# Performance work log

Measured on AMD Instinct MI355X. Metric: run time of the kernel, lower is better.

The kernel has to match this reference:

```python
import jax, jax.numpy as jnp
import numpy as np

H = 5  # hidden size of both LSTMs

def _lstm_layer(x, Wih, Whh, bih, bhh):
    """x: [B,T,I] -> hs: [B,T,H]. PyTorch gate order i,f,g,o; zero init state."""
    B, T, _ = x.shape
    # precompute input contribution for all timesteps: [T,B,4H]
    xg = (jnp.einsum('bti,gi->btg', x, Wih) + bih + bhh).transpose(1, 0, 2)
    def step(carry, xg_t):
        h, c = carry
        g = xg_t + h @ Whh.T
        i, f, gg, o = jnp.split(g, 4, axis=-1)
        c = jax.nn.sigmoid(f) * c + jax.nn.sigmoid(i) * jnp.tanh(gg)
        h = jax.nn.sigmoid(o) * jnp.tanh(c)
        return (h, c), h
    h0 = jnp.zeros((B, H), x.dtype)
    (_, _), hs = jax.lax.scan(step, (h0, h0), xg)
    return hs.transpose(1, 0, 2)  # [B,T,H]

def setup_inputs() -> dict:
    key = jax.random.key(0)
    ks = jax.random.split(key, 32)
    B, T = 16384, 128
    def u(k, shape, fan):
        s = 1.0 / np.sqrt(fan)
        return jax.random.uniform(k, shape, jnp.float32, -s, s)
    inp = {
        'x1': jax.random.normal(ks[0], (B, T, 5), jnp.float32),
        'x2': jax.random.normal(ks[1], (B, T, 5), jnp.float32),
        # lstm1 (1 layer)
        'Wih1': u(ks[2], (4*H, 5), H), 'Whh1': u(ks[3], (4*H, H), H),
        'bih1': u(ks[4], (4*H,), H), 'bhh1': u(ks[5], (4*H,), H),
        # lstm2 layer 0
        'Wih2a': u(ks[6], (4*H, 5), H), 'Whh2a': u(ks[7], (4*H, H), H),
        'bih2a': u(ks[8], (4*H,), H), 'bhh2a': u(ks[9], (4*H,), H),
        # lstm2 layer 1
        'Wih2b': u(ks[10], (4*H, H), H), 'Whh2b': u(ks[11], (4*H, H), H),
        'bih2b': u(ks[12], (4*H,), H), 'bhh2b': u(ks[13], (4*H,), H),
        # FC stack 20->32->32->16->16->5
        'W1': u(ks[14], (32, 20), 20), 'b1': u(ks[15], (32,), 20),
        'W2': u(ks[16], (32, 32), 32), 'b2': u(ks[17], (32,), 32),
        'W3': u(ks[18], (16, 32), 32), 'b3': u(ks[19], (16,), 32),
        'W4': u(ks[20], (16, 16), 16), 'b4': u(ks[21], (16,), 16),
        'W5': u(ks[22], (5, 16), 16), 'b5': u(ks[23], (5,), 16),
    }
    return inp

def reference(x1, x2, Wih1, Whh1, bih1, bhh1, Wih2a, Whh2a, bih2a, bhh2a,
              Wih2b, Whh2b, bih2b, bhh2b, W1, b1, W2, b2, W3, b3, W4, b4, W5, b5):
    out1 = _lstm_layer(x1, Wih1, Whh1, bih1, bhh1)[:, -1, :]            # [B,5]
    h2 = _lstm_layer(x2, Wih2a, Whh2a, bih2a, bhh2a)                    # [B,T,5]
    out2 = _lstm_layer(h2, Wih2b, Whh2b, bih2b, bhh2b)[:, -1, :]        # [B,5]
    out = jnp.concatenate([x1[:, -1, :], x2[:, -1, :], out1, out2], axis=1)  # [B,20]
    out = jax.nn.relu(out @ W1.T + b1)
    out = jax.nn.relu(out @ W2.T + b2)
    out = jax.nn.relu(out @ W3.T + b3)
    out = jax.nn.relu(out @ W4.T + b4)
    return out @ W5.T + b5  # [B,5]
```

## Files before the change

### kernel.cpp

```cpp
#include <hip/hip_runtime.h>

#define DEV __device__ __forceinline__
#define KSIG (-1.442695041f)
#define KTANH (-2.885390082f)

typedef float f2 __attribute__((ext_vector_type(2)));
typedef float f4 __attribute__((ext_vector_type(4)));

DEV float fexp2(float x) { return __builtin_amdgcn_exp2f(x); }
DEV float frcp(float x) { return __builtin_amdgcn_rcpf(x); }
DEV float bperm(int a, float x) {
  return __int_as_float(__builtin_amdgcn_ds_bpermute(a, __float_as_int(x)));
}
DEV f2 pkfma(f2 a, f2 b, f2 c) { return __builtin_elementwise_fma(a, b, c); }

struct CellP {
  f2 wx[4][2];
  f2 wh[4][2];
  float wx4[4], wh4[4];
  f2 b2[4];
};

DEV void load_cellP(CellP& W, int u, const float* __restrict__ Wih,
                    const float* __restrict__ Whh,
                    const float* __restrict__ bih,
                    const float* __restrict__ bhh) {
#pragma unroll
  for (int rt = 0; rt < 4; ++rt) {
    int row = 5 * rt + u;
    float kx = (rt == 2) ? KTANH : KSIG;
    W.wx[rt][0] = (f2){kx * Wih[row * 5 + 0], kx * Wih[row * 5 + 1]};
    W.wx[rt][1] = (f2){kx * Wih[row * 5 + 2], kx * Wih[row * 5 + 3]};
    W.wx4[rt] = kx * Wih[row * 5 + 4];
    W.wh[rt][0] = (f2){kx * Whh[row * 5 + 0], kx * Whh[row * 5 + 1]};
    W.wh[rt][1] = (f2){kx * Whh[row * 5 + 2], kx * Whh[row * 5 + 3]};
    W.wh4[rt] = kx * Whh[row * 5 + 4];
    W.b2[rt] = (f2){kx * (bih[row] + bhh[row]), 0.f};
  }
}

DEV float stepP(const CellP& W, const f2 xp[2], float x4, float hAll[5],
                float& c, const int bp[5]) {
  f2 hp0 = (f2){hAll[0], hAll[1]};
  f2 hp1 = (f2){hAll[2], hAll[3]};
  float acc[4];
#pragma unroll
  for (int rt = 0; rt < 4; ++rt) {
    f2 a2 = pkfma(W.wh[rt][0], hp0, W.b2[rt]);
    a2 = pkfma(W.wh[rt][1], hp1, a2);
    a2 = pkfma(W.wx[rt][0], xp[0], a2);
    a2 = pkfma(W.wx[rt][1], xp[1], a2);
    float a = a2.x + a2.y;
    a = fmaf(W.wh4[rt], hAll[4], a);
    acc[rt] = fmaf(W.wx4[rt], x4, a);
  }
  float gi = frcp(1.f + fexp2(acc[0]));
  float gf = frcp(1.f + fexp2(acc[1]));
  float gg = fmaf(2.f, frcp(1.f + fexp2(acc[2])), -1.f);
  float go = frcp(1.f + fexp2(acc[3]));
  c = fmaf(gf, c, gi * gg);
  float th = fmaf(2.f, frcp(1.f + fexp2(KTANH * c)), -1.f);
  float h = go * th;
#pragma unroll
  for (int u2 = 0; u2 < 5; ++u2) hAll[u2] = bperm(bp[u2], h);
  return h;
}

struct XBuf {
  f4 a, b, c, d, e;
};
DEV void xload(XBuf& bf, const float* __restrict__ px, int ch) {
  const f4* q = (const f4*)px + ch * 5;
  bf.a = q[0];
  bf.b = q[1];
  bf.c = q[2];
  bf.d = q[3];
  bf.e = q[4];
}

__global__ __launch_bounds__(192, 3) void rnn_a_kernel(
    const float* __restrict__ x1, const float* __restrict__ x2,
    const float* __restrict__ Wih1, const float* __restrict__ Whh1,
    const float* __restrict__ bih1, const float* __restrict__ bhh1,
    const float* __restrict__ Wih2a, const float* __restrict__ Whh2a,
    const float* __restrict__ bih2a, const float* __restrict__ bhh2a,
    float* __restrict__ h2a, float* __restrict__ h1l, int B, int N1) {
  const int tid = threadIdx.x;
  const int wid = blockIdx.x * 3 + (tid >> 6);
  if (wid >= 2 * N1) return;
  const int l = tid & 63;
  int g = l / 5;
  const int u = l - 5 * g;
  const bool act = (g < 12);
  if (!act) g = 11;
  const bool r2 = (wid >= N1);
  const int e = (r2 ? wid - N1 : wid) * 12 + g;
  const int ec = (e < B) ? e : B - 1;

  CellP W;
  if (r2)
    load_cellP(W, u, Wih2a, Whh2a, bih2a, bhh2a);
  else
    load_cellP(W, u, Wih1, Whh1, bih1, bhh1);

  int bp[5];
#pragma unroll
  for (int k = 0; k < 5; ++k) bp[k] = (5 * g + k) * 4;

  const float* px = (r2 ? x2 : x1) + (size_t)ec * 640;
  const bool wr = r2 && act && (e < B);
  float* ps = h2a + (size_t)ec * 640 + u;

  float hAll[5];
  float c = 0.f, hOwn = 0.f;
#pragma unroll
  for (int k = 0; k < 5; ++k) hAll[k] = 0.f;

#define SA1(S, xa, xb, xc, xd, xe)                  \
  {                                                 \
    f2 xin[2] = {(f2){xa, xb}, (f2){xc, xd}};       \
    hOwn = stepP(W, xin, xe, hAll, c, bp);          \
    if (wr) pst[(S) * 5] = hOwn;                    \
  }
#define CHUNKA(X)                                  \
  SA1(0, X.a.x, X.a.y, X.a.z, X.a.w, X.b.x)        \
  SA1(1, X.b.y, X.b.z, X.b.w, X.c.x, X.c.y)        \
  SA1(2, X.c.z, X.c.w, X.d.x, X.d.y, X.d.z)        \
  SA1(3, X.d.w, X.e.x, X.e.y, X.e.z, X.e.w)

  XBuf A0, B0;
  xload(A0, px, 0);
  for (int ch = 0; ch < 32; ch += 2) {
    xload(B0, px, (ch + 1 < 32) ? ch + 1 : 31);
    {
      float* pst = ps + (size_t)ch * 20;
      CHUNKA(A0);
    }
    xload(A0, px, (ch + 2 < 32) ? ch + 2 : 31);
    {
      float* pst = ps + (size_t)(ch + 1) * 20;
      CHUNKA(B0);
    }
  }
#undef SA1
#undef CHUNKA

  if (!r2 && act && e < B) h1l[(size_t)e * 5 + u] = hOwn;
}

__global__ __launch_bounds__(192, 2) void rnn_b_kernel(
    const float* __restrict__ x1, const float* __restrict__ x2,
    const float* __restrict__ Wih2b, const float* __restrict__ Whh2b,
    const float* __restrict__ bih2b, const float* __restrict__ bhh2b,
    const float* __restrict__ W1, const float* __restrict__ b1,
    const float* __restrict__ W2, const float* __restrict__ b2,
    const float* __restrict__ W3, const float* __restrict__ b3,
    const float* __restrict__ W4, const float* __restrict__ b4,
    const float* __restrict__ W5, const float* __restrict__ b5,
    const float* __restrict__ h2a, const float* __restrict__ h1l,
    float* __restrict__ out, int B) {
  __shared__ float sIn[36][20];
  __shared__ float sA[36][32];
  __shared__ float sB[36][32];

  const int tid = threadIdx.x;
  const int w = tid >> 6;
  const int l = tid & 63;
  int g = l / 5;
  const int u = l - 5 * g;
  const bool act = (g < 12);
  if (!act) g = 11;
  const int el = w * 12 + g;
  const int e = blockIdx.x * 36 + el;
  const int ec = (e < B) ? e : B - 1;

  CellP W;
  load_cellP(W, u, Wih2b, Whh2b, bih2b, bhh2b);

  int bp[5];
#pragma unroll
  for (int k = 0; k < 5; ++k) bp[k] = (5 * g + k) * 4;

  const float* ph = h2a + (size_t)ec * 640;

  float hAll[5];
  float c = 0.f, hOwn = 0.f;
#pragma unroll
  for (int k = 0; k < 5; ++k) hAll[k] = 0.f;

#define SB1(xa, xb, xc, xd, xe)                 \
  {                                             \
    f2 xin[2] = {(f2){xa, xb}, (f2){xc, xd}};   \
    hOwn = stepP(W, xin, xe, hAll, c, bp);      \
  }
#define CHUNKB(X)                              \
  SB1(X.a.x, X.a.y, X.a.z, X.a.w, X.b.x)       \
  SB1(X.b.y, X.b.z, X.b.w, X.c.x, X.c.y)       \
  SB1(X.c.z, X.c.w, X.d.x, X.d.y, X.d.z)       \
  SB1(X.d.w, X.e.x, X.e.y, X.e.z, X.e.w)

  XBuf A0, B0;
  xload(A0, ph, 0);
  for (int ch = 0; ch < 32; ch += 2) {
    xload(B0, ph, (ch + 1 < 32) ? ch + 1 : 31);
    CHUNKB(A0);
    xload(A0, ph, (ch + 2 < 32) ? ch + 2 : 31);
    CHUNKB(B0);
  }
#undef SB1
#undef CHUNKB

  if (act) {
    sIn[el][u] = x1[(size_t)ec * 640 + 635 + u];
    sIn[el][5 + u] = x2[(size_t)ec * 640 + 635 + u];
    sIn[el][10 + u] = h1l[(size_t)ec * 5 + u];
    sIn[el][15 + u] = hOwn;
  }
  __syncthreads();

  for (int task = tid; task < 36 * 32; task += 192) {
    int e2 = task >> 5, n = task & 31;
    float acc = b1[n];
#pragma unroll
    for (int k = 0; k < 20; ++k) acc = fmaf(W1[n * 20 + k], sIn[e2][k], acc);
    sA[e2][n] = fmaxf(acc, 0.f);
  }
  __syncthreads();
  for (int task = tid; task < 36 * 32; task += 192) {
    int e2 = task >> 5, n = task & 31;
    float acc = b2[n];
#pragma unroll
    for (int k = 0; k < 32; ++k) acc = fmaf(W2[n * 32 + k], sA[e2][k], acc);
    sB[e2][n] = fmaxf(acc, 0.f);
  }
  __syncthreads();
  for (int task = tid; task < 36 * 16; task += 192) {
    int e2 = task >> 4, n = task & 15;
    float acc = b3[n];
#pragma unroll
    for (int k = 0; k < 32; ++k) acc = fmaf(W3[n * 32 + k], sB[e2][k], acc);
    sA[e2][n] = fmaxf(acc, 0.f);
  }
  __syncthreads();
  for (int task = tid; task < 36 * 16; task += 192) {
    int e2 = task >> 4, n = task & 15;
    float acc = b4[n];
#pragma unroll
    for (int k = 0; k < 16; ++k) acc = fmaf(W4[n * 16 + k], sA[e2][k], acc);
    sB[e2][n] = fmaxf(acc, 0.f);
  }
  __syncthreads();
  for (int task = tid; task < 36 * 5; task += 192) {
    int e2 = task / 5, n = task - 5 * (task / 5);
    float acc = b5[n];
#pragma unroll
    for (int k = 0; k < 16; ++k) acc = fmaf(W5[n * 16 + k], sB[e2][k], acc);
    int ego = blockIdx.x * 36 + e2;
    if (ego < B) out[(size_t)ego * 5 + n] = acc;
  }
}

__global__ __launch_bounds__(192, 2) void rnn_stag_kernel(
    const float* __restrict__ x1, const float* __restrict__ x2,
    const float* __restrict__ Wih1, const float* __restrict__ Whh1,
    const float* __restrict__ bih1, const float* __restrict__ bhh1,
    const float* __restrict__ Wih2a, const float* __restrict__ Whh2a,
    const float* __restrict__ bih2a, const float* __restrict__ bhh2a,
    const float* __restrict__ Wih2b, const float* __restrict__ Whh2b,
    const float* __restrict__ bih2b, const float* __restrict__ bhh2b,
    const float* __restrict__ W1, const float* __restrict__ b1,
    const float* __restrict__ W2, const float* __restrict__ b2,
    const float* __restrict__ W3, const float* __restrict__ b3,
    const float* __restrict__ W4, const float* __restrict__ b4,
    const float* __restrict__ W5, const float* __restrict__ b5,
    float* __restrict__ out, int B) {
  __shared__ float sIn[24][20];
  __shared__ float sA[24][32];
  __shared__ float sB[24][32];

  const int tid = threadIdx.x;
  const int w = tid >> 6;
  const int l = tid & 63;
  int g = l / 5;
  const int u = l - 5 * g;
  const bool act = (g < 12);
  if (!act) g = 11;
  const int base = blockIdx.x * 24;

  int bp[5];
#pragma unroll
  for (int k = 0; k < 5; ++k) bp[k] = (5 * g + k) * 4;

  if (w == 0) {
    CellP W;
    load_cellP(W, u, Wih1, Whh1, bih1, bhh1);
    const int e0 = base + 2 * g, e1 = e0 + 1;
    const int e0c = (e0 < B) ? e0 : B - 1;
    const int e1c = (e1 < B) ? e1 : B - 1;
    const float* p0 = x1 + (size_t)e0c * 640;
    const float* p1 = x1 + (size_t)e1c * 640;
    float h0[5], h1[5];
    float c0 = 0.f, c1 = 0.f, ho0 = 0.f, ho1 = 0.f;
#pragma unroll
    for (int k = 0; k < 5; ++k) {
      h0[k] = 0.f;
      h1[k] = 0.f;
    }
    f2 xa[2] = {(f2){p0[0], p0[1]}, (f2){p0[2], p0[3]}};
    f2 xb[2] = {(f2){p1[0], p1[1]}, (f2){p1[2], p1[3]}};
    float xa4 = p0[4], xb4 = p1[4];
    for (int t = 0; t < 128; ++t) {
      f2 xia[2] = {xa[0], xa[1]}, xib[2] = {xb[0], xb[1]};
      float xia4 = xa4, xib4 = xb4;
      const int tn = (t < 127) ? t + 1 : 127;
      xa[0] = (f2){p0[tn * 5 + 0], p0[tn * 5 + 1]};
      xa[1] = (f2){p0[tn * 5 + 2], p0[tn * 5 + 3]};
      xa4 = p0[tn * 5 + 4];
      xb[0] = (f2){p1[tn * 5 + 0], p1[tn * 5 + 1]};
      xb[1] = (f2){p1[tn * 5 + 2], p1[tn * 5 + 3]};
      xb4 = p1[tn * 5 + 4];
      ho0 = stepP(W, xia, xia4, h0, c0, bp);
      ho1 = stepP(W, xib, xib4, h1, c1, bp);
    }
    if (act) {
      sIn[2 * g][u] = x1[(size_t)e0c * 640 + 635 + u];
      sIn[2 * g][10 + u] = ho0;
      sIn[2 * g + 1][u] = x1[(size_t)e1c * 640 + 635 + u];
      sIn[2 * g + 1][10 + u] = ho1;
    }
  } else {
    CellP Wa, Wb;
    load_cellP(Wa, u, Wih2a, Whh2a, bih2a, bhh2a);
    load_cellP(Wb, u, Wih2b, Whh2b, bih2b, bhh2b);
    const int el = ((w == 1) ? 0 : 12) + g;
    const int e = base + el;
    const int ec = (e < B) ? e : B - 1;
    const float* px = x2 + (size_t)ec * 640;
    float hA[5], hB[5];
    float cA = 0.f, cB = 0.f, hoB = 0.f;
#pragma unroll
    for (int k = 0; k < 5; ++k) {
      hA[k] = 0.f;
      hB[k] = 0.f;
    }
    f2 xc[2] = {(f2){px[0], px[1]}, (f2){px[2], px[3]}};
    float xc4 = px[4];
    (void)stepP(Wa, xc, xc4, hA, cA, bp);
    xc[0] = (f2){px[5], px[6]};
    xc[1] = (f2){px[7], px[8]};
    xc4 = px[9];
    for (int t = 1; t < 128; ++t) {
      f2 xin[2] = {xc[0], xc[1]};
      float xin4 = xc4;
      const int tn = (t < 127) ? t + 1 : 127;
      xc[0] = (f2){px[tn * 5 + 0], px[tn * 5 + 1]};
      xc[1] = (f2){px[tn * 5 + 2], px[tn * 5 + 3]};
      xc4 = px[tn * 5 + 4];
      f2 hin[2] = {(f2){hA[0], hA[1]}, (f2){hA[2], hA[3]}};
      float hin4 = hA[4];
      (void)stepP(Wa, xin, xin4, hA, cA, bp);
      hoB = stepP(Wb, hin, hin4, hB, cB, bp);
    }
    {
      f2 hin[2] = {(f2){hA[0], hA[1]}, (f2){hA[2], hA[3]}};
      hoB = stepP(Wb, hin, hA[4], hB, cB, bp);
    }
    if (act) {
      sIn[el][5 + u] = x2[(size_t)ec * 640 + 635 + u];
      sIn[el][15 + u] = hoB;
    }
  }
  __syncthreads();

  for (int task = tid; task < 24 * 32; task += 192) {
    int e = task >> 5, n = task & 31;
    float acc = b1[n];
#pragma unroll
    for (int k = 0; k < 20; ++k) acc = fmaf(W1[n * 20 + k], sIn[e][k], acc);
    sA[e][n] = fmaxf(acc, 0.f);
  }
  __syncthreads();
  for (int task = tid; task < 24 * 32; task += 192) {
    int e = task >> 5, n = task & 31;
    float acc = b2[n];
#pragma unroll
    for (int k = 0; k < 32; ++k) acc = fmaf(W2[n * 32 + k], sA[e][k], acc);
    sB[e][n] = fmaxf(acc, 0.f);
  }
  __syncthreads();
  for (int task = tid; task < 24 * 16; task += 192) {
    int e = task >> 4, n = task & 15;
    float acc = b3[n];
#pragma unroll
    for (int k = 0; k < 32; ++k) acc = fmaf(W3[n * 32 + k], sB[e][k], acc);
    sA[e][n] = fmaxf(acc, 0.f);
  }
  __syncthreads();
  for (int task = tid; task < 24 * 16; task += 192) {
    int e = task >> 4, n = task & 15;
    float acc = b4[n];
#pragma unroll
    for (int k = 0; k < 16; ++k) acc = fmaf(W4[n * 16 + k], sA[e][k], acc);
    sB[e][n] = fmaxf(acc, 0.f);
  }
  __syncthreads();
  if (tid < 120) {
    int e = tid / 5, n = tid - 5 * (tid / 5);
    float acc = b5[n];
#pragma unroll
    for (int k = 0; k < 16; ++k) acc = fmaf(W5[n * 16 + k], sB[e][k], acc);
    int ego = base + e;
    if (ego < B) out[(size_t)ego * 5 + n] = acc;
  }
}

extern "C" void kernel_launch(void* const* d_in, const int* in_sizes, int n_in,
                              void* d_out, int out_size, void* d_ws,
                              size_t ws_size, hipStream_t stream) {
  const float* x1 = (const float*)d_in[0];
  const float* x2 = (const float*)d_in[1];
  const float* Wih1 = (const float*)d_in[2];
  const float* Whh1 = (const float*)d_in[3];
  const float* bih1 = (const float*)d_in[4];
  const float* bhh1 = (const float*)d_in[5];
  const float* Wih2a = (const float*)d_in[6];
  const float* Whh2a = (const float*)d_in[7];
  const float* bih2a = (const float*)d_in[8];
  const float* bhh2a = (const float*)d_in[9];
  const float* Wih2b = (const float*)d_in[10];
  const float* Whh2b = (const float*)d_in[11];
  const float* bih2b = (const float*)d_in[12];
  const float* bhh2b = (const float*)d_in[13];
  const float* W1 = (const float*)d_in[14];
  const float* b1 = (const float*)d_in[15];
  const float* W2 = (const float*)d_in[16];
  const float* b2 = (const float*)d_in[17];
  const float* W3 = (const float*)d_in[18];
  const float* b3 = (const float*)d_in[19];
  const float* W4 = (const float*)d_in[20];
  const float* b4 = (const float*)d_in[21];
  const float* W5 = (const float*)d_in[22];
  const float* b5 = (const float*)d_in[23];

  int B = in_sizes[0] / 640;
  size_t req = ((size_t)B * 640 + (size_t)B * 5) * sizeof(float);

  if (d_ws && ws_size >= req) {
    float* h2a = (float*)d_ws;
    float* h1l = h2a + (size_t)B * 640;
    int N1 = (B + 11) / 12;
    int nA = (2 * N1 + 2) / 3;
    int nB = (B + 35) / 36;
    rnn_a_kernel<<<nA, 192, 0, stream>>>(x1, x2, Wih1, Whh1, bih1, bhh1, Wih2a,
                                         Whh2a, bih2a, bhh2a, h2a, h1l, B, N1);
    rnn_b_kernel<<<nB, 192, 0, stream>>>(x1, x2, Wih2b, Whh2b, bih2b, bhh2b,
                                         W1, b1, W2, b2, W3, b3, W4, b4, W5,
                                         b5, h2a, h1l, (float*)d_out, B);
  } else {
    int nB = (B + 23) / 24;
    rnn_stag_kernel<<<nB, 192, 0, stream>>>(
        x1, x2, Wih1, Whh1, bih1, bhh1, Wih2a, Whh2a, bih2a, bhh2a, Wih2b,
        Whh2b, bih2b, bhh2b, W1, b1, W2, b2, W3, b3, W4, b4, W5, b5,
        (float*)d_out, B);
  }
}
```

Baseline: 242.0 us.

## Use single-wave blocks, scalar per-step prefetch, pinned weights and reordered gate sums

```diff
diff --git a/kernel.cpp b/kernel.cpp
--- a/kernel.cpp
+++ b/kernel.cpp
@@ -5,7 +5,6 @@
 #define KTANH (-2.885390082f)
 
 typedef float f2 __attribute__((ext_vector_type(2)));
-typedef float f4 __attribute__((ext_vector_type(4)));
 
 DEV float fexp2(float x) { return __builtin_amdgcn_exp2f(x); }
 DEV float frcp(float x) { return __builtin_amdgcn_rcpf(x); }
@@ -13,6 +12,13 @@
   return __int_as_float(__builtin_amdgcn_ds_bpermute(a, __float_as_int(x)));
 }
 DEV f2 pkfma(f2 a, f2 b, f2 c) { return __builtin_elementwise_fma(a, b, c); }
+
+DEV void pinf(float& x) { asm volatile("" : "+v"(x)); }
+DEV void pin2(f2& v) {
+  float a = v.x, b = v.y;
+  asm volatile("" : "+v"(a), "+v"(b));
+  v = (f2){a, b};
+}
 
 struct CellP {
   f2 wx[4][2];
@@ -37,6 +43,16 @@
     W.wh4[rt] = kx * Whh[row * 5 + 4];
     W.b2[rt] = (f2){kx * (bih[row] + bhh[row]), 0.f};
   }
+#pragma unroll
+  for (int rt = 0; rt < 4; ++rt) {
+    pin2(W.wx[rt][0]);
+    pin2(W.wx[rt][1]);
+    pin2(W.wh[rt][0]);
+    pin2(W.wh[rt][1]);
+    pin2(W.b2[rt]);
+    pinf(W.wx4[rt]);
+    pinf(W.wh4[rt]);
+  }
 }
 
 DEV float stepP(const CellP& W, const f2 xp[2], float x4, float hAll[5],
@@ -46,13 +62,13 @@
   float acc[4];
 #pragma unroll
   for (int rt = 0; rt < 4; ++rt) {
-    f2 a2 = pkfma(W.wh[rt][0], hp0, W.b2[rt]);
+    f2 a2 = pkfma(W.wx[rt][0], xp[0], W.b2[rt]);
+    a2 = pkfma(W.wx[rt][1], xp[1], a2);
+    float s = W.wx4[rt] * x4;
+    a2 = pkfma(W.wh[rt][0], hp0, a2);
     a2 = pkfma(W.wh[rt][1], hp1, a2);
-    a2 = pkfma(W.wx[rt][0], xp[0], a2);
-    a2 = pkfma(W.wx[rt][1], xp[1], a2);
-    float a = a2.x + a2.y;
-    a = fmaf(W.wh4[rt], hAll[4], a);
-    acc[rt] = fmaf(W.wx4[rt], x4, a);
+    s = fmaf(W.wh4[rt], hAll[4], s);
+    acc[rt] = a2.x + a2.y + s;
   }
   float gi = frcp(1.f + fexp2(acc[0]));
   float gf = frcp(1.f + fexp2(acc[1]));
@@ -66,35 +82,20 @@
   return h;
 }
 
-struct XBuf {
-  f4 a, b, c, d, e;
-};
-DEV void xload(XBuf& bf, const float* __restrict__ px, int ch) {
-  const f4* q = (const f4*)px + ch * 5;
-  bf.a = q[0];
-  bf.b = q[1];
-  bf.c = q[2];
-  bf.d = q[3];
-  bf.e = q[4];
-}
-
-__global__ __launch_bounds__(192, 3) void rnn_a_kernel(
+__global__ __launch_bounds__(64, 4) void rnn_a_kernel(
     const float* __restrict__ x1, const float* __restrict__ x2,
     const float* __restrict__ Wih1, const float* __restrict__ Whh1,
     const float* __restrict__ bih1, const float* __restrict__ bhh1,
     const float* __restrict__ Wih2a, const float* __restrict__ Whh2a,
     const float* __restrict__ bih2a, const float* __restrict__ bhh2a,
     float* __restrict__ h2a, float* __restrict__ h1l, int B, int N1) {
-  const int tid = threadIdx.x;
-  const int wid = blockIdx.x * 3 + (tid >> 6);
-  if (wid >= 2 * N1) return;
-  const int l = tid & 63;
+  const int l = threadIdx.x;
   int g = l / 5;
   const int u = l - 5 * g;
   const bool act = (g < 12);
   if (!act) g = 11;
-  const bool r2 = (wid >= N1);
-  const int e = (r2 ? wid - N1 : wid) * 12 + g;
+  const bool r2 = (blockIdx.x >= N1);
+  const int e = (r2 ? blockIdx.x - N1 : blockIdx.x) * 12 + g;
   const int ec = (e < B) ? e : B - 1;
 
   CellP W;
@@ -116,39 +117,23 @@
 #pragma unroll
   for (int k = 0; k < 5; ++k) hAll[k] = 0.f;
 
-#define SA1(S, xa, xb, xc, xd, xe)                  \
-  {                                                 \
-    f2 xin[2] = {(f2){xa, xb}, (f2){xc, xd}};       \
-    hOwn = stepP(W, xin, xe, hAll, c, bp);          \
-    if (wr) pst[(S) * 5] = hOwn;                    \
-  }
-#define CHUNKA(X)                                  \
-  SA1(0, X.a.x, X.a.y, X.a.z, X.a.w, X.b.x)        \
-  SA1(1, X.b.y, X.b.z, X.b.w, X.c.x, X.c.y)        \
-  SA1(2, X.c.z, X.c.w, X.d.x, X.d.y, X.d.z)        \
-  SA1(3, X.d.w, X.e.x, X.e.y, X.e.z, X.e.w)
-
-  XBuf A0, B0;
-  xload(A0, px, 0);
-  for (int ch = 0; ch < 32; ch += 2) {
-    xload(B0, px, (ch + 1 < 32) ? ch + 1 : 31);
-    {
-      float* pst = ps + (size_t)ch * 20;
-      CHUNKA(A0);
-    }
-    xload(A0, px, (ch + 2 < 32) ? ch + 2 : 31);
-    {
-      float* pst = ps + (size_t)(ch + 1) * 20;
-      CHUNKA(B0);
-    }
-  }
-#undef SA1
-#undef CHUNKA
+  f2 xp[2] = {(f2){px[0], px[1]}, (f2){px[2], px[3]}};
+  float x4 = px[4];
+  for (int t = 0; t < 128; ++t) {
+    f2 xi[2] = {xp[0], xp[1]};
+    float xi4 = x4;
+    const int tn = (t < 127) ? t + 1 : 127;
+    xp[0] = (f2){px[tn * 5 + 0], px[tn * 5 + 1]};
+    xp[1] = (f2){px[tn * 5 + 2], px[tn * 5 + 3]};
+    x4 = px[tn * 5 + 4];
+    hOwn = stepP(W, xi, xi4, hAll, c, bp);
+    if (wr) ps[t * 5] = hOwn;
+  }
 
   if (!r2 && act && e < B) h1l[(size_t)e * 5 + u] = hOwn;
 }
 
-__global__ __launch_bounds__(192, 2) void rnn_b_kernel(
+__global__ __launch_bounds__(64, 4) void rnn_b_kernel(
     const float* __restrict__ x1, const float* __restrict__ x2,
     const float* __restrict__ Wih2b, const float* __restrict__ Whh2b,
     const float* __restrict__ bih2b, const float* __restrict__ bhh2b,
@@ -159,19 +144,16 @@
     const float* __restrict__ W5, const float* __restrict__ b5,
     const float* __restrict__ h2a, const float* __restrict__ h1l,
     float* __restrict__ out, int B) {
-  __shared__ float sIn[36][20];
-  __shared__ float sA[36][32];
-  __shared__ float sB[36][32];
-
-  const int tid = threadIdx.x;
-  const int w = tid >> 6;
-  const int l = tid & 63;
+  __shared__ float sIn[12][20];
+  __shared__ float sA[12][32];
+  __shared__ float sB[12][32];
+
+  const int l = threadIdx.x;
   int g = l / 5;
   const int u = l - 5 * g;
   const bool act = (g < 12);
   if (!act) g = 11;
-  const int el = w * 12 + g;
-  const int e = blockIdx.x * 36 + el;
+  const int e = blockIdx.x * 12 + g;
   const int ec = (e < B) ? e : B - 1;
 
   CellP W;
@@ -188,37 +170,27 @@
 #pragma unroll
   for (int k = 0; k < 5; ++k) hAll[k] = 0.f;
 
-#define SB1(xa, xb, xc, xd, xe)                 \
-  {                                             \
-    f2 xin[2] = {(f2){xa, xb}, (f2){xc, xd}};   \
-    hOwn = stepP(W, xin, xe, hAll, c, bp);      \
-  }
-#define CHUNKB(X)                              \
-  SB1(X.a.x, X.a.y, X.a.z, X.a.w, X.b.x)       \
-  SB1(X.b.y, X.b.z, X.b.w, X.c.x, X.c.y)       \
-  SB1(X.c.z, X.c.w, X.d.x, X.d.y, X.d.z)       \
-  SB1(X.d.w, X.e.x, X.e.y, X.e.z, X.e.w)
-
-  XBuf A0, B0;
-  xload(A0, ph, 0);
-  for (int ch = 0; ch < 32; ch += 2) {
-    xload(B0, ph, (ch + 1 < 32) ? ch + 1 : 31);
-    CHUNKB(A0);
-    xload(A0, ph, (ch + 2 < 32) ? ch + 2 : 31);
-    CHUNKB(B0);
-  }
-#undef SB1
-#undef CHUNKB
+  f2 xp[2] = {(f2){ph[0], ph[1]}, (f2){ph[2], ph[3]}};
+  float x4 = ph[4];
+  for (int t = 0; t < 128; ++t) {
+    f2 xi[2] = {xp[0], xp[1]};
+    float xi4 = x4;
+    const int tn = (t < 127) ? t + 1 : 127;
+    xp[0] = (f2){ph[tn * 5 + 0], ph[tn * 5 + 1]};
+    xp[1] = (f2){ph[tn * 5 + 2], ph[tn * 5 + 3]};
+    x4 = ph[tn * 5 + 4];
+    hOwn = stepP(W, xi, xi4, hAll, c, bp);
+  }
 
   if (act) {
-    sIn[el][u] = x1[(size_t)ec * 640 + 635 + u];
-    sIn[el][5 + u] = x2[(size_t)ec * 640 + 635 + u];
-    sIn[el][10 + u] = h1l[(size_t)ec * 5 + u];
-    sIn[el][15 + u] = hOwn;
-  }
-  __syncthreads();
-
-  for (int task = tid; task < 36 * 32; task += 192) {
+    sIn[g][u] = x1[(size_t)ec * 640 + 635 + u];
+    sIn[g][5 + u] = x2[(size_t)ec * 640 + 635 + u];
+    sIn[g][10 + u] = h1l[(size_t)ec * 5 + u];
+    sIn[g][15 + u] = hOwn;
+  }
+  __syncthreads();
+
+  for (int task = l; task < 12 * 32; task += 64) {
     int e2 = task >> 5, n = task & 31;
     float acc = b1[n];
 #pragma unroll
@@ -226,7 +198,7 @@
     sA[e2][n] = fmaxf(acc, 0.f);
   }
   __syncthreads();
-  for (int task = tid; task < 36 * 32; task += 192) {
+  for (int task = l; task < 12 * 32; task += 64) {
     int e2 = task >> 5, n = task & 31;
     float acc = b2[n];
 #pragma unroll
@@ -234,7 +206,7 @@
     sB[e2][n] = fmaxf(acc, 0.f);
   }
   __syncthreads();
-  for (int task = tid; task < 36 * 16; task += 192) {
+  for (int task = l; task < 12 * 16; task += 64) {
     int e2 = task >> 4, n = task & 15;
     float acc = b3[n];
 #pragma unroll
@@ -242,7 +214,7 @@
     sA[e2][n] = fmaxf(acc, 0.f);
   }
   __syncthreads();
-  for (int task = tid; task < 36 * 16; task += 192) {
+  for (int task = l; task < 12 * 16; task += 64) {
     int e2 = task >> 4, n = task & 15;
     float acc = b4[n];
 #pragma unroll
@@ -250,12 +222,12 @@
     sB[e2][n] = fmaxf(acc, 0.f);
   }
   __syncthreads();
-  for (int task = tid; task < 36 * 5; task += 192) {
-    int e2 = task / 5, n = task - 5 * (task / 5);
+  if (l < 60) {
+    int e2 = l / 5, n = l - 5 * (l / 5);
     float acc = b5[n];
 #pragma unroll
     for (int k = 0; k < 16; ++k) acc = fmaf(W5[n * 16 + k], sB[e2][k], acc);
-    int ego = blockIdx.x * 36 + e2;
+    int ego = blockIdx.x * 12 + e2;
     if (ego < B) out[(size_t)ego * 5 + n] = acc;
   }
 }
@@ -449,13 +421,12 @@
     float* h2a = (float*)d_ws;
     float* h1l = h2a + (size_t)B * 640;
     int N1 = (B + 11) / 12;
-    int nA = (2 * N1 + 2) / 3;
-    int nB = (B + 35) / 36;
-    rnn_a_kernel<<<nA, 192, 0, stream>>>(x1, x2, Wih1, Whh1, bih1, bhh1, Wih2a,
-                                         Whh2a, bih2a, bhh2a, h2a, h1l, B, N1);
-    rnn_b_kernel<<<nB, 192, 0, stream>>>(x1, x2, Wih2b, Whh2b, bih2b, bhh2b,
-                                         W1, b1, W2, b2, W3, b3, W4, b4, W5,
-                                         b5, h2a, h1l, (float*)d_out, B);
+    rnn_a_kernel<<<2 * N1, 64, 0, stream>>>(x1, x2, Wih1, Whh1, bih1, bhh1,
+                                            Wih2a, Whh2a, bih2a, bhh2a, h2a,
+                                            h1l, B, N1);
+    rnn_b_kernel<<<N1, 64, 0, stream>>>(x1, x2, Wih2b, Whh2b, bih2b, bhh2b, W1,
+                                        b1, W2, b2, W3, b3, W4, b4, W5, b5,
+                                        h2a, h1l, (float*)d_out, B);
   } else {
     int nB = (B + 23) / 24;
     rnn_stag_kernel<<<nB, 192, 0, stream>>>(
```

New measurement: 269.9 us. 1.12x slower.
